# Optimization experiments

Hardware: AMD Instinct MI355X
Metric: run time of the kernel (lower is better)

Reference implementation:

```python
import jax, jax.numpy as jnp
import numpy as np

EPS = 1e-5
B = 32


def _conv(x, w, b, s):
    y = jax.lax.conv_general_dilated(x, w, (s, s), 'VALID',
                                     dimension_numbers=('NCHW', 'OIHW', 'NCHW'))
    return y + b[None, :, None, None]


def _bn(x, g, b):
    # BatchNorm2d in training mode: per-batch statistics over (N,H,W)
    m = jnp.mean(x, axis=(0, 2, 3), keepdims=True)
    v = jnp.var(x, axis=(0, 2, 3), keepdims=True)
    return (x - m) * jax.lax.rsqrt(v + EPS) * g[None, :, None, None] + b[None, :, None, None]


def _pool(x):
    # MaxPool2d(3, stride=2), no padding
    return jax.lax.reduce_window(x, -jnp.inf, jax.lax.max,
                                 (1, 1, 3, 3), (1, 1, 2, 2), 'VALID')


def _backbone(x, p):
    x = _pool(jax.nn.relu(_bn(_conv(x, p['conv1_w'], p['conv1_b'], 2), p['bn1_g'], p['bn1_b'])))
    x = _pool(jax.nn.relu(_bn(_conv(x, p['conv2_w'], p['conv2_b'], 1), p['bn2_g'], p['bn2_b'])))
    x = jax.nn.relu(_bn(_conv(x, p['conv3_w'], p['conv3_b'], 1), p['bn3_g'], p['bn3_b']))
    x = jax.nn.relu(_bn(_conv(x, p['conv4_w'], p['conv4_b'], 1), p['bn4_g'], p['bn4_b']))
    x = _bn(_conv(x, p['conv5_w'], p['conv5_b'], 1), p['bn5_g'], p['bn5_b'])
    return x


def _forward(input1, input2, p):
    o1 = _backbone(input1, p)  # [B, 128, 22, 22]
    o2 = _backbone(input2, p)  # [B, 128, 6, 6]
    b, c, h, w = o1.shape
    # The torch loop sums over batch AND channels at each (i,j), then divides
    # by output2.nelement() (= B*C*6*6). Equivalent: one valid cross-correlation
    # with B*C input channels producing a single [1,1,oH,oW] map, broadcast to B.
    corr = jax.lax.conv_general_dilated(
        o1.reshape(1, b * c, h, w),
        o2.reshape(1, b * c, o2.shape[2], o2.shape[3]),
        (1, 1), 'VALID', dimension_numbers=('NCHW', 'OIHW', 'NCHW'))
    corr = corr / o2.size
    return jnp.broadcast_to(corr, (b, 1, corr.shape[2], corr.shape[3]))


def setup_inputs() -> dict:
    key = jax.random.key(0)
    ks = jax.random.split(key, 8)
    d = {}
    d['input1'] = jax.random.normal(ks[0], (B, 3, 255, 255), jnp.float32)
    d['input2'] = jax.random.normal(ks[1], (B, 3, 127, 127), jnp.float32)
    conv_shapes = {'conv1_w': (96, 3, 11, 11), 'conv2_w': (256, 96, 5, 5),
                   'conv3_w': (192, 256, 3, 3), 'conv4_w': (192, 192, 3, 3),
                   'conv5_w': (128, 192, 3, 3)}
    for i, (name, sh) in enumerate(conv_shapes.items()):
        fan_out = sh[0] * sh[2] * sh[3]  # kaiming_normal_ fan_out, relu gain
        d[name] = jax.random.normal(ks[2 + i], sh, jnp.float32) * np.sqrt(2.0 / fan_out).astype(np.float32)
        d[name.replace('_w', '_b')] = jnp.zeros((sh[0],), jnp.float32)
    for name, c in {'bn1': 96, 'bn2': 256, 'bn3': 192, 'bn4': 192, 'bn5': 128}.items():
        d[name + '_g'] = jnp.ones((c,), jnp.float32)
        d[name + '_b'] = jnp.zeros((c,), jnp.float32)
    return d


def reference(input1, input2, conv1_w, conv1_b, bn1_g, bn1_b,
              conv2_w, conv2_b, bn2_g, bn2_b,
              conv3_w, conv3_b, bn3_g, bn3_b,
              conv4_w, conv4_b, bn4_g, bn4_b,
              conv5_w, conv5_b, bn5_g, bn5_b):
    p = dict(conv1_w=conv1_w, conv1_b=conv1_b, bn1_g=bn1_g, bn1_b=bn1_b,
             conv2_w=conv2_w, conv2_b=conv2_b, bn2_g=bn2_g, bn2_b=bn2_b,
             conv3_w=conv3_w, conv3_b=conv3_b, bn3_g=bn3_g, bn3_b=bn3_b,
             conv4_w=conv4_w, conv4_b=conv4_b, bn4_g=bn4_g, bn4_b=bn4_b,
             conv5_w=conv5_w, conv5_b=conv5_b, bn5_g=bn5_g, bn5_b=bn5_b)
    return _forward(input1, input2, p)
```

## Files before the change

kernel.cpp:

```cpp
#include <hip/hip_runtime.h>
#include <hip/hip_bf16.h>
#include <cstdint>
#include <cstddef>

typedef __attribute__((ext_vector_type(8))) _Float16 f16x8;
typedef __attribute__((ext_vector_type(4))) float f32x4;

__device__ __forceinline__ float h2f(unsigned short u) {
  union { unsigned short s; _Float16 h; } x; x.s = u; return (float)x.h;
}
__device__ __forceinline__ unsigned short f2h(float f) {
  union { unsigned short s; _Float16 h; } x; x.h = (_Float16)f; return x.s;
}
__device__ __forceinline__ void gload_lds16(const void* g, void* l) {
  __builtin_amdgcn_global_load_lds((const __attribute__((address_space(1))) unsigned int*)g,
                                   (__attribute__((address_space(3))) unsigned int*)l, 16, 0, 0);
}

__global__ void in_all(const float* __restrict__ in1, const float* __restrict__ in2,
                       unsigned short* __restrict__ o1, unsigned short* __restrict__ o2) {
  int i = blockIdx.x * 256 + threadIdx.x;
  const int p1 = 32 * 255 * 255;
  const int p2 = 32 * 127 * 127;
  const float* in;
  unsigned short* o;
  int HW;
  if (i < p1) {
    in = in1; o = o1; HW = 255 * 255;
  } else if (i < p1 + p2) {
    i -= p1; in = in2; o = o2; HW = 127 * 127;
  } else return;
  int n = i / HW;
  int r = i - n * HW;
  const float* p = in + (long)n * 3 * HW + r;
  uint2 v;
  v.x = (unsigned)f2h(p[0]) | ((unsigned)f2h(p[HW]) << 16);
  v.y = (unsigned)f2h(p[2 * HW]);
  ((uint2*)o)[i] = v;
}

__device__ __forceinline__ void wtx(const float* __restrict__ w, unsigned short* __restrict__ o,
                                    long i, int Co, int Co_pad, int Ci, int KK) {
  int ci = (int)(i % Ci);
  long r = i / Ci;
  int co = (int)(r % Co_pad);
  int rk = (int)(r / Co_pad);
  float v = 0.f;
  if (co < Co) v = w[((long)co * Ci + ci) * KK + rk];
  o[i] = f2h(v);
}
__global__ void wt_all(const float* __restrict__ w1, const float* __restrict__ w2,
                       const float* __restrict__ w3, const float* __restrict__ w4,
                       const float* __restrict__ w5,
                       unsigned short* __restrict__ W1h, unsigned short* __restrict__ W2,
                       unsigned short* __restrict__ W3, unsigned short* __restrict__ W4,
                       unsigned short* __restrict__ W5) {
  long i = (long)blockIdx.x * 256 + threadIdx.x;
  const long t1 = 17 * 128 * 32;
  const long t2 = 25l * 256 * 96;
  const long t3 = 9l * 256 * 256;
  const long t4 = 9l * 256 * 192;
  const long t5 = 9l * 128 * 192;
  if (i < t1) {
    int j = (int)(i & 31);
    int r = (int)(i >> 5);
    int co = r & 127;
    int kk = r >> 7;
    int run = kk * 4 + (j >> 3);
    int ky = run / 6;
    int e = (run - ky * 6) * 8 + (j & 7);
    int kx = e >> 2, c = e & 3;
    float v = 0.f;
    if (ky < 11 && kx < 11 && c < 3 && co < 96)
      v = w1[((co * 3 + c) * 11 + ky) * 11 + kx];
    W1h[i] = f2h(v);
  } else if (i < t1 + t2) {
    wtx(w2, W2, i - t1, 256, 256, 96, 25);
  } else if (i < t1 + t2 + t3) {
    wtx(w3, W3, i - t1 - t2, 192, 256, 256, 9);
  } else if (i < t1 + t2 + t3 + t4) {
    wtx(w4, W4, i - t1 - t2 - t3, 192, 256, 192, 9);
  } else if (i < t1 + t2 + t3 + t4 + t5) {
    wtx(w5, W5, i - t1 - t2 - t3 - t4, 128, 128, 192, 9);
  }
}

__global__ __launch_bounds__(256)
void conv1_mfma(const unsigned short* __restrict__ in, const unsigned short* __restrict__ wt,
                unsigned short* __restrict__ out, float* __restrict__ part,
                int Hi1, int Ho1, int NPIX1, int BX1, long inOff2, long outOff2,
                int Hi2, int Ho2, int NPIX2) {
  __shared__ __align__(16) unsigned short sA[2][128 * 32];
  __shared__ __align__(16) unsigned short sB[2][128 * 32];
  __shared__ int sOB[128];
  __shared__ float sRed[4][64][2];
  const int t = threadIdx.x;
  const int bxg = blockIdx.x;
  const bool br2 = bxg >= BX1;
  const int lbx = br2 ? bxg - BX1 : bxg;
  const unsigned short* inB = in + (br2 ? inOff2 : 0);
  unsigned short* outB = out + (br2 ? outOff2 : 0);
  const int Hi = br2 ? Hi2 : Hi1, Wi = Hi;
  const int Ho = br2 ? Ho2 : Ho1, Wo = Ho;
  const int NPIX = br2 ? NPIX2 : NPIX1;
  const int px0 = lbx * 128;
  if (t < 128) {
    int g = px0 + t;
    int ob = -1;
    if (g < NPIX) {
      int n = g / (Ho * Wo);
      int r = g - n * Ho * Wo;
      int oy = r / Wo, ox = r - (r / Wo) * Wo;
      ob = ((n * Ho + oy) * Wo + ox) * 96;
    }
    sOB[t] = ob;
  }
  long rbase[2];
#pragma unroll
  for (int i = 0; i < 2; ++i) {
    int pxl = i * 64 + (t >> 2);
    int g = px0 + pxl;
    long rb = 0;
    if (g < NPIX) {
      int n = g / (Ho * Wo);
      int r = g - n * Ho * Wo;
      int oy = r / Wo, ox = r - (r / Wo) * Wo;
      rb = ((long)(n * Hi + 2 * oy) * Wi + 2 * ox) * 4;
    }
    rbase[i] = rb;
  }
  const int swz = (t & 3) ^ ((t >> 3) & 3);
  const int W4 = Wi * 4;
  f32x4 acc[4][4];
  f32x4 zz = {0.f, 0.f, 0.f, 0.f};
#pragma unroll
  for (int m = 0; m < 4; ++m)
#pragma unroll
    for (int n = 0; n < 4; ++n) acc[m][n] = zz;
  const int w = t >> 6;
  const int l = t & 63;
  const int wpx = (w & 1) * 64, wco = (w >> 1) * 64;
  const int arow = wpx + (l & 15);
  const int brow = wco + (l & 15);
  const int q8s = (((l >> 4) ^ (((l & 15) >> 1) & 3)) * 8);

  auto stage = [&](int buf, int kk) {
    int run = kk * 4 + swz;
    int ky = run / 6;
    int e0 = (run - ky * 6) * 8;
    long koff = (long)ky * W4 + e0;
    gload_lds16(inB + rbase[0] + koff, &sA[buf][t * 8]);
    gload_lds16(inB + rbase[1] + koff, &sA[buf][(256 + t) * 8]);
    const unsigned short* wp = wt + (long)kk * 4096;
    gload_lds16(wp + (t >> 2) * 32 + swz * 8, &sB[buf][t * 8]);
    gload_lds16(wp + 2048 + (t >> 2) * 32 + swz * 8, &sB[buf][(256 + t) * 8]);
  };

  stage(0, 0);
  __syncthreads();
  int cur = 0;
#pragma unroll 1
  for (int kk = 0; kk < 17; ++kk) {
    if (kk + 1 < 17) stage(cur ^ 1, kk + 1);
    f16x8 av[4], bv[4];
#pragma unroll
    for (int m = 0; m < 4; ++m) av[m] = *(const f16x8*)&sA[cur][(arow + m * 16) * 32 + q8s];
#pragma unroll
    for (int n = 0; n < 4; ++n) bv[n] = *(const f16x8*)&sB[cur][(brow + n * 16) * 32 + q8s];
#pragma unroll
    for (int m = 0; m < 4; ++m)
#pragma unroll
      for (int n = 0; n < 4; ++n)
        acc[m][n] = __builtin_amdgcn_mfma_f32_16x16x32_f16(av[m], bv[n], acc[m][n], 0, 0, 0);
    __syncthreads();
    cur ^= 1;
  }
#pragma unroll
  for (int m = 0; m < 4; ++m) {
#pragma unroll
    for (int r = 0; r < 4; ++r) {
      int pxl = wpx + m * 16 + (l >> 4) * 4 + r;
      int ob = sOB[pxl];
#pragma unroll
      for (int n = 0; n < 4; ++n) {
        int co = wco + n * 16 + (l & 15);
        if (ob >= 0 && co < 96) outB[ob + co] = f2h(acc[m][n][r]);
      }
    }
  }
  float sn[4], qn[4];
#pragma unroll
  for (int n = 0; n < 4; ++n) { sn[n] = 0.f; qn[n] = 0.f; }
#pragma unroll
  for (int m = 0; m < 4; ++m) {
#pragma unroll
    for (int r = 0; r < 4; ++r) {
      int pxl = wpx + m * 16 + (l >> 4) * 4 + r;
      float msk = (px0 + pxl < NPIX) ? 1.f : 0.f;
#pragma unroll
      for (int n = 0; n < 4; ++n) {
        float v = acc[m][n][r] * msk;
        sn[n] += v;
        qn[n] = fmaf(v, v, qn[n]);
      }
    }
  }
#pragma unroll
  for (int n = 0; n < 4; ++n) {
    sn[n] += __shfl_xor(sn[n], 16, 64);
    sn[n] += __shfl_xor(sn[n], 32, 64);
    qn[n] += __shfl_xor(qn[n], 16, 64);
    qn[n] += __shfl_xor(qn[n], 32, 64);
  }
  if (l < 16) {
#pragma unroll
    for (int n = 0; n < 4; ++n) {
      sRed[w][n * 16 + l][0] = sn[n];
      sRed[w][n * 16 + l][1] = qn[n];
    }
  }
  __syncthreads();
  if (t < 128) {
    int wb = (t >> 6) << 1;
    int cl = t & 63;
    float S = sRed[wb][cl][0] + sRed[wb + 1][cl][0];
    float Q = sRed[wb][cl][1] + sRed[wb + 1][cl][1];
    long idx = ((long)t * gridDim.x + bxg) * 2;
    part[idx] = S;
    part[idx + 1] = Q;
  }
}

template <int K>
__global__ __launch_bounds__(256)
void conv_mfma(const unsigned short* __restrict__ in, const unsigned short* __restrict__ wt,
               unsigned short* __restrict__ out, float* __restrict__ part,
               int Ci, int Co_pad, int Co_real,
               int Hi1, int Ho1, int NPIX1, int BX1, long inOff2, long outOff2,
               int Hi2, int Ho2, int NPIX2) {
  __shared__ __align__(16) unsigned short sA[2][128 * 32];
  __shared__ __align__(16) unsigned short sB[2][128 * 32];
  __shared__ int sOB[128];
  __shared__ float sRed[4][64][2];
  const int t = threadIdx.x;
  const int bxg = blockIdx.x;
  const bool br2 = bxg >= BX1;
  const int lbx = br2 ? bxg - BX1 : bxg;
  const unsigned short* inB = in + (br2 ? inOff2 : 0);
  unsigned short* outB = out + (br2 ? outOff2 : 0);
  const int Hi = br2 ? Hi2 : Hi1, Wi = Hi;
  const int Ho = br2 ? Ho2 : Ho1, Wo = Ho;
  const int NPIX = br2 ? NPIX2 : NPIX1;
  const int px0 = lbx * 128;
  const int co0 = blockIdx.y * 128;
  if (t < 128) {
    int g = px0 + t;
    int ob = -1;
    if (g < NPIX) {
      int n = g / (Ho * Wo);
      int r = g - n * Ho * Wo;
      int oy = r / Wo, ox = r - (r / Wo) * Wo;
      ob = ((n * Ho + oy) * Wo + ox) * Co_real;
    }
    sOB[t] = ob;
  }
  long rbase[2];
#pragma unroll
  for (int i = 0; i < 2; ++i) {
    int pxl = i * 64 + (t >> 2);
    int g = px0 + pxl;
    long rb = 0;
    if (g < NPIX) {
      int n = g / (Ho * Wo);
      int r = g - n * Ho * Wo;
      int oy = r / Wo, ox = r - (r / Wo) * Wo;
      rb = ((long)(n * Hi + oy) * Wi + ox) * Ci;
    }
    rbase[i] = rb;
  }
  const int seg8 = ((t & 3) ^ ((t >> 3) & 3)) * 8;
  const int colA = t >> 2;
  f32x4 acc[4][4];
  f32x4 zz = {0.f, 0.f, 0.f, 0.f};
#pragma unroll
  for (int m = 0; m < 4; ++m)
#pragma unroll
    for (int n = 0; n < 4; ++n) acc[m][n] = zz;
  const int w = t >> 6;
  const int l = t & 63;
  const int wpx = (w & 1) * 64, wco = (w >> 1) * 64;
  const int arow = wpx + (l & 15);
  const int brow = wco + (l & 15);
  const int q8s = (((l >> 4) ^ (((l & 15) >> 1) & 3)) * 8);
  int ci0 = 0, kx = 0, ky = 0;
  const int NK = (Ci >> 5) * K * K;

  auto stage = [&](int buf) {
    long koff = (long)(ky * Wi + kx) * Ci + ci0 + seg8;
    gload_lds16(inB + rbase[0] + koff, &sA[buf][t * 8]);
    gload_lds16(inB + rbase[1] + koff, &sA[buf][(256 + t) * 8]);
    long wbase = (long)((ky * K + kx) * Co_pad + co0) * Ci + ci0 + seg8;
    gload_lds16(wt + wbase + (long)colA * Ci, &sB[buf][t * 8]);
    gload_lds16(wt + wbase + (long)(64 + colA) * Ci, &sB[buf][(256 + t) * 8]);
    ci0 += 32;
    if (ci0 == Ci) { ci0 = 0; ++kx; if (kx == K) { kx = 0; ++ky; } }
  };

  stage(0);
  __syncthreads();
  int cur = 0;
#pragma unroll 1
  for (int kk = 0; kk < NK; ++kk) {
    if (kk + 1 < NK) stage(cur ^ 1);
    f16x8 av[4], bv[4];
#pragma unroll
    for (int m = 0; m < 4; ++m) av[m] = *(const f16x8*)&sA[cur][(arow + m * 16) * 32 + q8s];
#pragma unroll
    for (int n = 0; n < 4; ++n) bv[n] = *(const f16x8*)&sB[cur][(brow + n * 16) * 32 + q8s];
#pragma unroll
    for (int m = 0; m < 4; ++m)
#pragma unroll
      for (int n = 0; n < 4; ++n)
        acc[m][n] = __builtin_amdgcn_mfma_f32_16x16x32_f16(av[m], bv[n], acc[m][n], 0, 0, 0);
    __syncthreads();
    cur ^= 1;
  }
#pragma unroll
  for (int m = 0; m < 4; ++m) {
#pragma unroll
    for (int r = 0; r < 4; ++r) {
      int pxl = wpx + m * 16 + (l >> 4) * 4 + r;
      int ob = sOB[pxl];
#pragma unroll
      for (int n = 0; n < 4; ++n) {
        int co = co0 + wco + n * 16 + (l & 15);
        if (ob >= 0 && co < Co_real) outB[ob + co] = f2h(acc[m][n][r]);
      }
    }
  }
  float sn[4], qn[4];
#pragma unroll
  for (int n = 0; n < 4; ++n) { sn[n] = 0.f; qn[n] = 0.f; }
#pragma unroll
  for (int m = 0; m < 4; ++m) {
#pragma unroll
    for (int r = 0; r < 4; ++r) {
      int pxl = wpx + m * 16 + (l >> 4) * 4 + r;
      float msk = (px0 + pxl < NPIX) ? 1.f : 0.f;
#pragma unroll
      for (int n = 0; n < 4; ++n) {
        float v = acc[m][n][r] * msk;
        sn[n] += v;
        qn[n] = fmaf(v, v, qn[n]);
      }
    }
  }
#pragma unroll
  for (int n = 0; n < 4; ++n) {
    sn[n] += __shfl_xor(sn[n], 16, 64);
    sn[n] += __shfl_xor(sn[n], 32, 64);
    qn[n] += __shfl_xor(qn[n], 16, 64);
    qn[n] += __shfl_xor(qn[n], 32, 64);
  }
  if (l < 16) {
#pragma unroll
    for (int n = 0; n < 4; ++n) {
      sRed[w][n * 16 + l][0] = sn[n];
      sRed[w][n * 16 + l][1] = qn[n];
    }
  }
  __syncthreads();
  if (t < 128) {
    int wb = (t >> 6) << 1;
    int cl = t & 63;
    float S = sRed[wb][cl][0] + sRed[wb + 1][cl][0];
    float Q = sRed[wb][cl][1] + sRed[wb + 1][cl][1];
    long idx = ((long)(co0 + t) * gridDim.x + bxg) * 2;
    part[idx] = S;
    part[idx + 1] = Q;
  }
}

__global__ void bn_finalize(const float* __restrict__ part, const float* __restrict__ g,
                            const float* __restrict__ b, float* __restrict__ sc,
                            float* __restrict__ sh, int C, int BX1, int BXtot,
                            float cnt1, float cnt2) {
  const int cb = blockIdx.x;
  const bool br2 = cb >= C;
  const int c = br2 ? cb - C : cb;
  const int k0 = br2 ? BX1 : 0;
  const int k1 = br2 ? BXtot : BX1;
  const float cnt = br2 ? cnt2 : cnt1;
  const int t = threadIdx.x;
  float s = 0.f, q = 0.f;
  const float* pc = part + (long)c * BXtot * 2;
  for (int k = k0 + t; k < k1; k += 256) {
    s += pc[k * 2];
    q += pc[k * 2 + 1];
  }
  __shared__ float ss[256], qq[256];
  ss[t] = s; qq[t] = q;
  __syncthreads();
  for (int off = 128; off > 0; off >>= 1) {
    if (t < off) { ss[t] += ss[t + off]; qq[t] += qq[t + off]; }
    __syncthreads();
  }
  if (t == 0) {
    float m = ss[0] / cnt;
    float v = qq[0] / cnt - m * m;
    float r = rsqrtf(v + 1e-5f);
    float scl = r * g[c];
    int o = c + (br2 ? 256 : 0);
    sc[o] = scl;
    sh[o] = b[c] - m * scl;
  }
}

template <bool RELU, bool OUTF32>
__global__ void bn_apply_k(const unsigned short* __restrict__ x, void* __restrict__ y,
                           const float* __restrict__ sc, const float* __restrict__ sh,
                           int C, long t81, long t82, long xOff2, long yOff2q4) {
  long i = (long)blockIdx.x * blockDim.x + threadIdx.x;
  if (i >= t81 + t82) return;
  const bool br2 = i >= t81;
  const long ii = br2 ? i - t81 : i;
  const int scO = br2 ? 256 : 0;
  const uint4 v = ((const uint4*)x + (br2 ? xOff2 : 0))[ii];
  int c0 = (int)((ii * 8) % C);
  const float4 s0 = *(const float4*)&sc[scO + c0];
  const float4 s1 = *(const float4*)&sc[scO + c0 + 4];
  const float4 h0 = *(const float4*)&sh[scO + c0];
  const float4 h1 = *(const float4*)&sh[scO + c0 + 4];
  float f[8];
  f[0] = h2f((unsigned short)(v.x & 0xffff)); f[1] = h2f((unsigned short)(v.x >> 16));
  f[2] = h2f((unsigned short)(v.y & 0xffff)); f[3] = h2f((unsigned short)(v.y >> 16));
  f[4] = h2f((unsigned short)(v.z & 0xffff)); f[5] = h2f((unsigned short)(v.z >> 16));
  f[6] = h2f((unsigned short)(v.w & 0xffff)); f[7] = h2f((unsigned short)(v.w >> 16));
  const float S[8] = {s0.x, s0.y, s0.z, s0.w, s1.x, s1.y, s1.z, s1.w};
  const float H[8] = {h0.x, h0.y, h0.z, h0.w, h1.x, h1.y, h1.z, h1.w};
#pragma unroll
  for (int j = 0; j < 8; ++j) {
    f[j] = fmaf(f[j], S[j], H[j]);
    if (RELU) f[j] = fmaxf(f[j], 0.f);
  }
  if (OUTF32) {
    float4* yb = (float4*)y + (br2 ? yOff2q4 : 0);
    float4 o0 = {f[0], f[1], f[2], f[3]}, o1 = {f[4], f[5], f[6], f[7]};
    yb[2 * ii] = o0;
    yb[2 * ii + 1] = o1;
  } else {
    uint4 o;
    o.x = (unsigned)f2h(f[0]) | ((unsigned)f2h(f[1]) << 16);
    o.y = (unsigned)f2h(f[2]) | ((unsigned)f2h(f[3]) << 16);
    o.z = (unsigned)f2h(f[4]) | ((unsigned)f2h(f[5]) << 16);
    o.w = (unsigned)f2h(f[6]) | ((unsigned)f2h(f[7]) << 16);
    ((uint4*)y + (br2 ? xOff2 : 0))[ii] = o;
  }
}

__global__ void bn_pool_k(const unsigned short* __restrict__ in, unsigned short* __restrict__ out,
                          const float* __restrict__ sc, const float* __restrict__ sh,
                          int C8, int Hi1, int Ho1, long t81, long inOff2, long outOff2,
                          int Hi2, int Ho2, long t82) {
  long i = (long)blockIdx.x * blockDim.x + threadIdx.x;
  if (i >= t81 + t82) return;
  const bool br2 = i >= t81;
  const long ii = br2 ? i - t81 : i;
  const int Hi = br2 ? Hi2 : Hi1, Wi = Hi;
  const int Ho = br2 ? Ho2 : Ho1, Wo = Ho;
  const int scO = br2 ? 256 : 0;
  const uint4* inB = (const uint4*)in + (br2 ? inOff2 : 0);
  uint4* outB = (uint4*)out + (br2 ? outOff2 : 0);
  int cg = (int)(ii % C8);
  long r = ii / C8;
  int ox = (int)(r % Wo);
  r /= Wo;
  int oy = (int)(r % Ho);
  int n = (int)(r / Ho);
  const int c0 = cg * 8;
  const float4 s0 = *(const float4*)&sc[scO + c0];
  const float4 s1 = *(const float4*)&sc[scO + c0 + 4];
  const float4 h0 = *(const float4*)&sh[scO + c0];
  const float4 h1 = *(const float4*)&sh[scO + c0 + 4];
  const float S[8] = {s0.x, s0.y, s0.z, s0.w, s1.x, s1.y, s1.z, s1.w};
  const float H[8] = {h0.x, h0.y, h0.z, h0.w, h1.x, h1.y, h1.z, h1.w};
  const uint4* bp = inB + ((long)(n * Hi + 2 * oy) * Wi + 2 * ox) * C8 + cg;
  float m[8];
#pragma unroll
  for (int j = 0; j < 8; ++j) m[j] = -3.4e38f;
#pragma unroll
  for (int dy = 0; dy < 3; ++dy)
#pragma unroll
    for (int dx = 0; dx < 3; ++dx) {
      const uint4 v = bp[((long)dy * Wi + dx) * C8];
      float f[8];
      f[0] = h2f((unsigned short)(v.x & 0xffff)); f[1] = h2f((unsigned short)(v.x >> 16));
      f[2] = h2f((unsigned short)(v.y & 0xffff)); f[3] = h2f((unsigned short)(v.y >> 16));
      f[4] = h2f((unsigned short)(v.z & 0xffff)); f[5] = h2f((unsigned short)(v.z >> 16));
      f[6] = h2f((unsigned short)(v.w & 0xffff)); f[7] = h2f((unsigned short)(v.w >> 16));
#pragma unroll
      for (int j = 0; j < 8; ++j) {
        f[j] = fmaxf(fmaf(f[j], S[j], H[j]), 0.f);
        m[j] = fmaxf(m[j], f[j]);
      }
    }
  uint4 o;
  o.x = (unsigned)f2h(m[0]) | ((unsigned)f2h(m[1]) << 16);
  o.y = (unsigned)f2h(m[2]) | ((unsigned)f2h(m[3]) << 16);
  o.z = (unsigned)f2h(m[4]) | ((unsigned)f2h(m[5]) << 16);
  o.w = (unsigned)f2h(m[6]) | ((unsigned)f2h(m[7]) << 16);
  outB[ii] = o;
}

__global__ void xcorr_part(const float* __restrict__ o1, const float* __restrict__ o2,
                           float* __restrict__ part) {
  const int p = blockIdx.x;
  const int b = blockIdx.y;
  const int oy = p / 17, ox = p - (p / 17) * 17;
  const float* o1b = o1 + (long)b * 22 * 22 * 128;
  const float* o2b = o2 + (long)b * 4608;
  float acc = 0.f;
  for (int i = threadIdx.x; i < 4608; i += 256) {
    int c = i & 127;
    int r = i >> 7;
    int kx = r % 6, ky = r / 6;
    acc = fmaf(o1b[((oy + ky) * 22 + ox + kx) * 128 + c], o2b[i], acc);
  }
#pragma unroll
  for (int off = 32; off > 0; off >>= 1) acc += __shfl_down(acc, off, 64);
  __shared__ float sh[4];
  const int lane = threadIdx.x & 63, wid = threadIdx.x >> 6;
  if (lane == 0) sh[wid] = acc;
  __syncthreads();
  if (threadIdx.x == 0) part[p * 32 + b] = sh[0] + sh[1] + sh[2] + sh[3];
}

__global__ void xcorr_out(const float* __restrict__ part, float* __restrict__ out, int total) {
  int i = blockIdx.x * 256 + threadIdx.x;
  if (i >= total) return;
  int p = i % 289;
  float s = 0.f;
  for (int b = 0; b < 32; ++b) s += part[p * 32 + b];
  out[i] = s * (1.f / 147456.f);
}

extern "C" void kernel_launch(void* const* d_in, const int* in_sizes, int n_in,
                              void* d_out, int out_size, void* d_ws, size_t ws_size,
                              hipStream_t stream) {
  (void)in_sizes; (void)n_in; (void)ws_size; (void)out_size;
  const float* input1 = (const float*)d_in[0];
  const float* input2 = (const float*)d_in[1];
  const float* cw[5];
  const float* bg[5];
  const float* bb[5];
  for (int i = 0; i < 5; ++i) {
    cw[i] = (const float*)d_in[2 + 2 * i];
    bg[i] = (const float*)d_in[12 + 2 * i];
    bb[i] = (const float*)d_in[13 + 2 * i];
  }
  const int H1a = 123, P1a = 61, H2a = 57, P2a = 28, H3a = 26, H4a = 24, H5a = 22;
  const int H1b = 59, P1b = 29, H2b = 25, P2b = 12, H3b = 10, H4b = 8, H5b = 6;
  auto NP = [](int h) { return 32 * h * h; };
  const int NP1a = NP(H1a), NP1b = NP(H1b);
  const int NP2a = NP(H2a), NP2b = NP(H2b);
  const int NP3a = NP(H3a), NP3b = NP(H3b);
  const int NP4a = NP(H4a), NP4b = NP(H4b);
  const int NP5a = NP(H5a), NP5b = NP(H5b);
  auto BX = [](int np) { return (np + 127) / 128; };

  char* p = (char*)d_ws;
  auto alloc = [&](size_t bytes) {
    char* r = p;
    p += (bytes + 255) & ~(size_t)255;
    return r;
  };
  unsigned short* P = (unsigned short*)alloc(((size_t)NP1a + NP1b) * 96 * 2);
  unsigned short* R = (unsigned short*)alloc(((size_t)NP(P1a) + NP(P1b)) * 96 * 2);
  unsigned short* Q = (unsigned short*)alloc(((size_t)NP4a + NP4b) * 192 * 2);
  float* O12 = (float*)alloc(((size_t)NP5a + NP5b) * 128 * 4);
  unsigned short* I12h = (unsigned short*)alloc(((size_t)32 * 255 * 255 * 4 + (size_t)32 * 127 * 127 * 4) * 2 + 16384);
  unsigned short* W1h = (unsigned short*)alloc(17l * 128 * 32 * 2);
  unsigned short* W2 = (unsigned short*)alloc(25l * 256 * 96 * 2);
  unsigned short* W3 = (unsigned short*)alloc(9l * 256 * 256 * 2);
  unsigned short* W4 = (unsigned short*)alloc(9l * 256 * 192 * 2);
  unsigned short* W5 = (unsigned short*)alloc(9l * 128 * 192 * 2);
  float* part = (float*)alloc(9000000);
  float* sc = (float*)alloc(512 * 4);
  float* sh = (float*)alloc(512 * 4);
  float* O1 = O12;
  float* O2 = O12 + (size_t)NP5a * 128;

  {
    long wt_tot = 17l * 128 * 32 + 25l * 256 * 96 + 9l * 256 * 256 + 9l * 256 * 192 + 9l * 128 * 192;
    wt_all<<<(unsigned)((wt_tot + 255) / 256), 256, 0, stream>>>(cw[0], cw[1], cw[2], cw[3], cw[4],
                                                                 W1h, W2, W3, W4, W5);
    long in_tot = 32l * 255 * 255 + 32l * 127 * 127;
    in_all<<<(unsigned)((in_tot + 255) / 256), 256, 0, stream>>>(input1, input2, I12h,
                                                                 I12h + 32l * 255 * 255 * 4);
  }

  {
    int BX1 = BX(NP1a), BXt = BX1 + BX(NP1b);
    conv1_mfma<<<(unsigned)BXt, 256, 0, stream>>>(I12h, W1h, P, part,
        255, H1a, NP1a, BX1, 32l * 255 * 255 * 4, (long)NP1a * 96,
        127, H1b, NP1b);
    bn_finalize<<<192, 256, 0, stream>>>(part, bg[0], bb[0], sc, sh, 96, BX1, BXt,
                                         (float)NP1a, (float)NP1b);
    long t81 = (long)NP(P1a) * 96 / 8, t82 = (long)NP(P1b) * 96 / 8;
    bn_pool_k<<<(unsigned)((t81 + t82 + 255) / 256), 256, 0, stream>>>(
        P, R, sc, sh, 12, H1a, P1a, t81, (long)NP1a * 96 / 8, t81, H1b, P1b, t82);
  }
  {
    int BX1 = BX(NP2a), BXt = BX1 + BX(NP2b);
    dim3 g((unsigned)BXt, 2);
    conv_mfma<5><<<g, 256, 0, stream>>>(R, W2, P, part, 96, 256, 256,
        P1a, H2a, NP2a, BX1, (long)NP(P1a) * 96, (long)NP2a * 256,
        P1b, H2b, NP2b);
    bn_finalize<<<512, 256, 0, stream>>>(part, bg[1], bb[1], sc, sh, 256, BX1, BXt,
                                         (float)NP2a, (float)NP2b);
    long t81 = (long)NP(P2a) * 256 / 8, t82 = (long)NP(P2b) * 256 / 8;
    bn_pool_k<<<(unsigned)((t81 + t82 + 255) / 256), 256, 0, stream>>>(
        P, R, sc, sh, 32, H2a, P2a, t81, (long)NP2a * 256 / 8, t81, H2b, P2b, t82);
  }
  {
    int BX1 = BX(NP3a), BXt = BX1 + BX(NP3b);
    dim3 g((unsigned)BXt, 2);
    conv_mfma<3><<<g, 256, 0, stream>>>(R, W3, P, part, 256, 256, 192,
        P2a, H3a, NP3a, BX1, (long)NP(P2a) * 256, (long)NP3a * 192,
        P2b, H3b, NP3b);
    bn_finalize<<<384, 256, 0, stream>>>(part, bg[2], bb[2], sc, sh, 192, BX1, BXt,
                                         (float)NP3a, (float)NP3b);
    long t81 = (long)NP3a * 192 / 8, t82 = (long)NP3b * 192 / 8;
    bn_apply_k<true, false><<<(unsigned)((t81 + t82 + 255) / 256), 256, 0, stream>>>(
        P, P, sc, sh, 192, t81, t82, t81, 0);
  }
  {
    int BX1 = BX(NP4a), BXt = BX1 + BX(NP4b);
    dim3 g((unsigned)BXt, 2);
    conv_mfma<3><<<g, 256, 0, stream>>>(P, W4, Q, part, 192, 256, 192,
        H3a, H4a, NP4a, BX1, (long)NP3a * 192, (long)NP4a * 192,
        H3b, H4b, NP4b);
    bn_finalize<<<384, 256, 0, stream>>>(part, bg[3], bb[3], sc, sh, 192, BX1, BXt,
                                         (float)NP4a, (float)NP4b);
    long t81 = (long)NP4a * 192 / 8, t82 = (long)NP4b * 192 / 8;
    bn_apply_k<true, false><<<(unsigned)((t81 + t82 + 255) / 256), 256, 0, stream>>>(
        Q, Q, sc, sh, 192, t81, t82, t81, 0);
  }
  {
    int BX1 = BX(NP5a), BXt = BX1 + BX(NP5b);
    dim3 g((unsigned)BXt, 1);
    conv_mfma<3><<<g, 256, 0, stream>>>(Q, W5, P, part, 192, 128, 128,
        H4a, H5a, NP5a, BX1, (long)NP4a * 192, (long)NP5a * 128,
        H4b, H5b, NP5b);
    bn_finalize<<<256, 256, 0, stream>>>(part, bg[4], bb[4], sc, sh, 128, BX1, BXt,
                                         (float)NP5a, (float)NP5b);
    long t81 = (long)NP5a * 128 / 8, t82 = (long)NP5b * 128 / 8;
    bn_apply_k<false, true><<<(unsigned)((t81 + t82 + 255) / 256), 256, 0, stream>>>(
        P, O12, sc, sh, 128, t81, t82, t81, (long)NP5a * 128 / 4);
  }

  xcorr_part<<<dim3(289, 32), 256, 0, stream>>>(O1, O2, part);
  xcorr_out<<<(9248 + 255) / 256, 256, 0, stream>>>(part, (float*)d_out, 9248);
}
```

Baseline: 607.8 us.

## Add dedicated 256x256-tile conv2 kernel with flattened padded K layout

Replaces the generic templated conv for layer 2 with a dedicated 512-thread kernel. Each block computes a 256-pixel by 256-channel tile, so one block covers all output channels and the input tile is loaded once instead of per channel half. The conv2 weights are repacked into a flattened K dimension of 25*96 padded to 2432, staged in 64-wide K steps with a split double buffer to overlap loads with MFMA. The larger tile raises register and LDS use (one block per CU) and reads past the end of the padded K range, which is why the workspace buffers get extra padding.

```diff
diff --git a/kernel.cpp b/kernel.cpp
--- a/kernel.cpp
+++ b/kernel.cpp
@@ -5,6 +5,9 @@
 
 typedef __attribute__((ext_vector_type(8))) _Float16 f16x8;
 typedef __attribute__((ext_vector_type(4))) float f32x4;
+
+#define KPAD2 2432
+#define NT2 38
 
 __device__ __forceinline__ float h2f(unsigned short u) {
   union { unsigned short s; _Float16 h; } x; x.s = u; return (float)x.h;
@@ -57,7 +60,7 @@
                        unsigned short* __restrict__ W5) {
   long i = (long)blockIdx.x * 256 + threadIdx.x;
   const long t1 = 17 * 128 * 32;
-  const long t2 = 25l * 256 * 96;
+  const long t2 = 256l * KPAD2;
   const long t3 = 9l * 256 * 256;
   const long t4 = 9l * 256 * 192;
   const long t5 = 9l * 128 * 192;
@@ -75,7 +78,13 @@
       v = w1[((co * 3 + c) * 11 + ky) * 11 + kx];
     W1h[i] = f2h(v);
   } else if (i < t1 + t2) {
-    wtx(w2, W2, i - t1, 256, 256, 96, 25);
+    long ii = i - t1;
+    int co = (int)(ii / KPAD2);
+    int k = (int)(ii - (long)co * KPAD2);
+    int e = k / 96, ci = k - (k / 96) * 96;
+    float v = 0.f;
+    if (e < 25) v = w2[((long)co * 96 + ci) * 25 + e];
+    W2[ii] = f2h(v);
   } else if (i < t1 + t2 + t3) {
     wtx(w3, W3, i - t1 - t2, 192, 256, 256, 9);
   } else if (i < t1 + t2 + t3 + t4) {
@@ -228,6 +237,179 @@
     long idx = ((long)t * gridDim.x + bxg) * 2;
     part[idx] = S;
     part[idx + 1] = Q;
+  }
+}
+
+__global__ __launch_bounds__(512, 1)
+void conv2_big(const unsigned short* __restrict__ in, const unsigned short* __restrict__ wt,
+               unsigned short* __restrict__ out, float* __restrict__ part,
+               int Hi1, int Ho1, int NPIX1, int BX1, long inOff2, long outOff2,
+               int Hi2, int Ho2, int NPIX2) {
+  __shared__ __align__(16) unsigned short sA[2][2][256 * 32];
+  __shared__ __align__(16) unsigned short sB[2][2][256 * 32];
+  __shared__ int sOB[256];
+  __shared__ float sRed[8][64][2];
+  const int t = threadIdx.x;
+  const int bxg = blockIdx.x;
+  const bool br2 = bxg >= BX1;
+  const int lbx = br2 ? bxg - BX1 : bxg;
+  const unsigned short* inB = in + (br2 ? inOff2 : 0);
+  unsigned short* outB = out + (br2 ? outOff2 : 0);
+  const int Hi = br2 ? Hi2 : Hi1, Wi = Hi;
+  const int Ho = br2 ? Ho2 : Ho1, Wo = Ho;
+  const int NPIX = br2 ? NPIX2 : NPIX1;
+  const int px0 = lbx * 256;
+  if (t < 256) {
+    int g = px0 + t;
+    int ob = -1;
+    if (g < NPIX) {
+      int n = g / (Ho * Wo);
+      int r = g - n * Ho * Wo;
+      int oy = r / Wo, ox = r - (r / Wo) * Wo;
+      ob = ((n * Ho + oy) * Wo + ox) * 256;
+    }
+    sOB[t] = ob;
+  }
+  long rbase[2];
+#pragma unroll
+  for (int j = 0; j < 2; ++j) {
+    int row = (t >> 2) + j * 128;
+    int g = px0 + row;
+    long rb = 0;
+    if (g < NPIX) {
+      int n = g / (Ho * Wo);
+      int r = g - n * Ho * Wo;
+      int oy = r / Wo, ox = r - (r / Wo) * Wo;
+      rb = ((long)(n * Hi + oy) * Wi + ox) * 96;
+    }
+    rbase[j] = rb;
+  }
+  const int w = t >> 6;
+  const int l = t & 63;
+  const int wr = w >> 2;
+  const int wc = w & 3;
+  f32x4 acc[8][4];
+  f32x4 zz = {0.f, 0.f, 0.f, 0.f};
+#pragma unroll
+  for (int m = 0; m < 8; ++m)
+#pragma unroll
+    for (int n = 0; n < 4; ++n) acc[m][n] = zz;
+
+  const int kseg = (t & 3) * 8;
+  const int bco = t >> 2;
+
+  auto stage = [&](int tile, int half, int buf) {
+    int k = tile * 64 + half * 32 + kseg;
+    int e = k / 96;
+    int ci = k - e * 96;
+    int ky = e / 5, kx = e - ky * 5;
+    long koff = (long)(ky * Wi + kx) * 96 + ci;
+    unsigned short* dA = &sA[buf][half][t * 8];
+    gload_lds16(inB + rbase[0] + koff, dA);
+    gload_lds16(inB + rbase[1] + koff, dA + 4096);
+    const unsigned short* ws = wt + (long)bco * KPAD2 + k;
+    unsigned short* dB = &sB[buf][half][t * 8];
+    gload_lds16(ws, dB);
+    gload_lds16(ws + 128l * KPAD2, dB + 4096);
+  };
+
+  auto compute = [&](int buf, int half) {
+    const unsigned short* A = &sA[buf][half][0];
+    const unsigned short* B = &sB[buf][half][0];
+    f16x8 av[8], bv[4];
+#pragma unroll
+    for (int m = 0; m < 8; ++m)
+      av[m] = *(const f16x8*)&A[(wr * 128 + (l & 15) + m * 16) * 32 + (l >> 4) * 8];
+#pragma unroll
+    for (int n = 0; n < 4; ++n)
+      bv[n] = *(const f16x8*)&B[(wc * 64 + (l & 15) + n * 16) * 32 + (l >> 4) * 8];
+#pragma unroll
+    for (int m = 0; m < 8; ++m)
+#pragma unroll
+      for (int n = 0; n < 4; ++n)
+        acc[m][n] = __builtin_amdgcn_mfma_f32_16x16x32_f16(av[m], bv[n], acc[m][n], 0, 0, 0);
+  };
+
+  stage(0, 0, 0);
+  stage(0, 1, 0);
+  stage(1, 0, 1);
+  asm volatile("s_waitcnt vmcnt(4) lgkmcnt(0)" ::: "memory");
+  __builtin_amdgcn_sched_barrier(0);
+  __builtin_amdgcn_s_barrier();
+  __builtin_amdgcn_sched_barrier(0);
+#pragma unroll 1
+  for (int tt = 0; tt < NT2; ++tt) {
+    const int b = tt & 1;
+    const int s1 = (tt + 1 < NT2) ? tt + 1 : NT2 - 1;
+    const int s2 = (tt + 2 < NT2) ? tt + 2 : NT2 - 1;
+    stage(s1, 1, b ^ 1);
+    compute(b, 0);
+    asm volatile("s_waitcnt vmcnt(8)" ::: "memory");
+    __builtin_amdgcn_sched_barrier(0);
+    __builtin_amdgcn_s_barrier();
+    __builtin_amdgcn_sched_barrier(0);
+    stage(s2, 0, b);
+    compute(b, 1);
+    asm volatile("s_waitcnt vmcnt(8)" ::: "memory");
+    __builtin_amdgcn_sched_barrier(0);
+    __builtin_amdgcn_s_barrier();
+    __builtin_amdgcn_sched_barrier(0);
+  }
+#pragma unroll
+  for (int m = 0; m < 8; ++m) {
+#pragma unroll
+    for (int r = 0; r < 4; ++r) {
+      int row = wr * 128 + m * 16 + (l >> 4) * 4 + r;
+      int ob = sOB[row];
+      if (ob >= 0) {
+#pragma unroll
+        for (int n = 0; n < 4; ++n) {
+          int co = wc * 64 + n * 16 + (l & 15);
+          outB[ob + co] = f2h(acc[m][n][r]);
+        }
+      }
+    }
+  }
+  float sn[4], qn[4];
+#pragma unroll
+  for (int n = 0; n < 4; ++n) { sn[n] = 0.f; qn[n] = 0.f; }
+#pragma unroll
+  for (int m = 0; m < 8; ++m) {
+#pragma unroll
+    for (int r = 0; r < 4; ++r) {
+      int row = wr * 128 + m * 16 + (l >> 4) * 4 + r;
+      float msk = (px0 + row < NPIX) ? 1.f : 0.f;
+#pragma unroll
+      for (int n = 0; n < 4; ++n) {
+        float v = acc[m][n][r] * msk;
+        sn[n] += v;
+        qn[n] = fmaf(v, v, qn[n]);
+      }
+    }
+  }
+#pragma unroll
+  for (int n = 0; n < 4; ++n) {
+    sn[n] += __shfl_xor(sn[n], 16, 64);
+    sn[n] += __shfl_xor(sn[n], 32, 64);
+    qn[n] += __shfl_xor(qn[n], 16, 64);
+    qn[n] += __shfl_xor(qn[n], 32, 64);
+  }
+  if (l < 16) {
+#pragma unroll
+    for (int n = 0; n < 4; ++n) {
+      sRed[w][n * 16 + l][0] = sn[n];
+      sRed[w][n * 16 + l][1] = qn[n];
+    }
+  }
+  __syncthreads();
+  if (t < 256) {
+    int wcg = t >> 6;
+    int idx = t & 63;
+    float S = sRed[wcg][idx][0] + sRed[wcg + 4][idx][0];
+    float Q = sRed[wcg][idx][1] + sRed[wcg + 4][idx][1];
+    long o = ((long)t * gridDim.x + bxg) * 2;
+    part[o] = S;
+    part[o + 1] = Q;
   }
 }
 
@@ -575,12 +757,12 @@
     return r;
   };
   unsigned short* P = (unsigned short*)alloc(((size_t)NP1a + NP1b) * 96 * 2);
-  unsigned short* R = (unsigned short*)alloc(((size_t)NP(P1a) + NP(P1b)) * 96 * 2);
+  unsigned short* R = (unsigned short*)alloc(((size_t)NP(P1a) + NP(P1b)) * 96 * 2 + 262144);
   unsigned short* Q = (unsigned short*)alloc(((size_t)NP4a + NP4b) * 192 * 2);
   float* O12 = (float*)alloc(((size_t)NP5a + NP5b) * 128 * 4);
-  unsigned short* I12h = (unsigned short*)alloc(((size_t)32 * 255 * 255 * 4 + (size_t)32 * 127 * 127 * 4) * 2 + 16384);
+  unsigned short* I12h = (unsigned short*)alloc(((size_t)32 * 255 * 255 * 4 + (size_t)32 * 127 * 127 * 4) * 2 + 65536);
   unsigned short* W1h = (unsigned short*)alloc(17l * 128 * 32 * 2);
-  unsigned short* W2 = (unsigned short*)alloc(25l * 256 * 96 * 2);
+  unsigned short* W2 = (unsigned short*)alloc(256l * KPAD2 * 2);
   unsigned short* W3 = (unsigned short*)alloc(9l * 256 * 256 * 2);
   unsigned short* W4 = (unsigned short*)alloc(9l * 256 * 192 * 2);
   unsigned short* W5 = (unsigned short*)alloc(9l * 128 * 192 * 2);
@@ -591,7 +773,7 @@
   float* O2 = O12 + (size_t)NP5a * 128;
 
   {
-    long wt_tot = 17l * 128 * 32 + 25l * 256 * 96 + 9l * 256 * 256 + 9l * 256 * 192 + 9l * 128 * 192;
+    long wt_tot = 17l * 128 * 32 + 256l * KPAD2 + 9l * 256 * 256 + 9l * 256 * 192 + 9l * 128 * 192;
     wt_all<<<(unsigned)((wt_tot + 255) / 256), 256, 0, stream>>>(cw[0], cw[1], cw[2], cw[3], cw[4],
                                                                  W1h, W2, W3, W4, W5);
     long in_tot = 32l * 255 * 255 + 32l * 127 * 127;
@@ -611,9 +793,8 @@
         P, R, sc, sh, 12, H1a, P1a, t81, (long)NP1a * 96 / 8, t81, H1b, P1b, t82);
   }
   {
-    int BX1 = BX(NP2a), BXt = BX1 + BX(NP2b);
-    dim3 g((unsigned)BXt, 2);
-    conv_mfma<5><<<g, 256, 0, stream>>>(R, W2, P, part, 96, 256, 256,
+    int BX1 = (NP2a + 255) / 256, BXt = BX1 + (NP2b + 255) / 256;
+    conv2_big<<<(unsigned)BXt, 512, 0, stream>>>(R, W2, P, part,
         P1a, H2a, NP2a, BX1, (long)NP(P1a) * 96, (long)NP2a * 256,
         P1b, H2b, NP2b);
     bn_finalize<<<512, 256, 0, stream>>>(part, bg[1], bb[1], sc, sh, 256, BX1, BXt,
```

Result: no change. 619.9 us (+2.0%).
